# Optimization experiments

Measured on AMD Instinct MI355X. Metric: run time of the kernel, lower is better.

Reference implementation:

```python
import jax, jax.numpy as jnp
import numpy as np

NUM_HEADS = 16
HEAD_DIM = 80
HIDDEN = 1280
SEQ = 3072
NUM_SEGS = 6  # 6 packed images of 512 patches each


def rotate_half(x):
    x1, x2 = jnp.split(x, 2, axis=-1)
    return jnp.concatenate([-x2, x1], axis=-1)


def setup_inputs() -> dict:
    key = jax.random.key(0)
    ks = jax.random.split(key, 6)
    hidden_states = jax.random.normal(ks[0], (SEQ, HIDDEN), dtype=jnp.float32)
    # RoPE tables as in Qwen-VL vision: freqs over half the head_dim, duplicated
    half = HEAD_DIM // 2
    inv_freq = 1.0 / (10000.0 ** (jnp.arange(half, dtype=jnp.float32) / half))
    pos = jnp.arange(SEQ, dtype=jnp.float32)[:, None]
    freqs = pos * inv_freq[None, :]                      # (SEQ, half)
    emb = jnp.concatenate([freqs, freqs], axis=-1)       # (SEQ, HEAD_DIM)
    cos = jnp.cos(emb)
    sin = jnp.sin(emb)
    # Packed segment boundaries: [0, 512, 1024, ..., 3072]
    cu_seqlens = jnp.arange(0, SEQ + 1, SEQ // NUM_SEGS, dtype=jnp.int32)
    scale = 0.02
    w_qkv = jax.random.normal(ks[1], (3 * HIDDEN, HIDDEN), dtype=jnp.float32) * scale
    b_qkv = jax.random.normal(ks[2], (3 * HIDDEN,), dtype=jnp.float32) * scale
    w_proj = jax.random.normal(ks[3], (HIDDEN, HIDDEN), dtype=jnp.float32) * scale
    b_proj = jax.random.normal(ks[4], (HIDDEN,), dtype=jnp.float32) * scale
    return {
        "hidden_states": hidden_states, "cos": cos, "sin": sin,
        "w_qkv": w_qkv, "b_qkv": b_qkv, "w_proj": w_proj, "b_proj": b_proj,
        "cu_seqlens": cu_seqlens,
    }


def reference(hidden_states, cos, sin, w_qkv, b_qkv, w_proj, b_proj, cu_seqlens):
    S, H = hidden_states.shape
    nh, hd = NUM_HEADS, H // NUM_HEADS

    # Fused QKV projection: (S, 3H) -> q, k, v each (S, nh, hd)
    qkv = hidden_states @ w_qkv.T + b_qkv
    qkv = qkv.reshape(S, 3, nh, hd)
    q, k, v = qkv[:, 0], qkv[:, 1], qkv[:, 2]

    # Inline RoPE on q/k (cos/sin broadcast over heads)
    c = cos[:, None, :]
    s = sin[:, None, :]
    q = q * c + rotate_half(q) * s
    k = k * c + rotate_half(k) * s

    # Original casts fp32 -> fp16 for the flash attention kernel
    q16 = q.astype(jnp.float16)
    k16 = k.astype(jnp.float16)
    v16 = v.astype(jnp.float16)

    # Varlen masking: tokens attend only within their own packed segment
    tok = jnp.arange(S)
    seg = jnp.searchsorted(cu_seqlens, tok, side="right")  # (S,)
    same_seg = seg[:, None] == seg[None, :]                 # (S, S)

    scale = hd ** (-0.5)
    # Scores accumulated in fp32 (as flash attention does internally)
    scores = jnp.einsum("qhd,khd->hqk", q16, k16,
                        preferred_element_type=jnp.float32) * scale
    scores = jnp.where(same_seg[None], scores, jnp.finfo(jnp.float32).min)
    weights = jax.nn.softmax(scores, axis=-1).astype(jnp.float16)  # (nh, S, S)

    attn = jnp.einsum("hqk,khd->qhd", weights, v16)  # (S, nh, hd) fp16
    attn = attn.astype(jnp.float32).reshape(S, H)
    return attn @ w_proj.T + b_proj
```

## Files before the change

kernel.cpp:

```cpp
#include <hip/hip_runtime.h>

typedef _Float16 f16;
typedef _Float16 half8 __attribute__((ext_vector_type(8)));
typedef _Float16 half4 __attribute__((ext_vector_type(4)));
typedef float f32x4 __attribute__((ext_vector_type(4)));

__device__ __forceinline__ void gld_lds16(const void* g, void* l) {
  __builtin_amdgcn_global_load_lds((const __attribute__((address_space(1))) void*)g,
                                   (__attribute__((address_space(3))) void*)l, 16, 0, 0);
}

template <int CTRL>
__device__ __forceinline__ float dppf(float x) {
  return __builtin_bit_cast(float,
      __builtin_amdgcn_mov_dpp(__builtin_bit_cast(int, x), CTRL, 0xf, 0xf, true));
}
__device__ __forceinline__ float dpp_max16(float v) {
  v = fmaxf(v, dppf<0xB1>(v));
  v = fmaxf(v, dppf<0x4E>(v));
  v = fmaxf(v, dppf<0x128>(v));
  v = fmaxf(v, dppf<0x140>(v));
  return v;
}
__device__ __forceinline__ float dpp_sum16(float v) {
  v += dppf<0xB1>(v);
  v += dppf<0x4E>(v);
  v += dppf<0x128>(v);
  v += dppf<0x140>(v);
  return v;
}

__global__ void cvt_all(const float* __restrict__ hid, const float* __restrict__ wq,
                        const float* __restrict__ wp, f16* __restrict__ hid16,
                        f16* __restrict__ wq16, f16* __restrict__ wp16) {
  int b = blockIdx.x;
  const float* in;
  f16* out;
  int i;
  if (b < 3840) { in = hid; out = hid16; i = b * 256 + threadIdx.x; }
  else if (b < 8640) { in = wq; out = wq16; i = (b - 3840) * 256 + threadIdx.x; }
  else { in = wp; out = wp16; i = (b - 8640) * 256 + threadIdx.x; }
  float4 v = ((const float4*)in)[i];
  half4 o;
  o.x = (f16)v.x; o.y = (f16)v.y; o.z = (f16)v.z; o.w = (f16)v.w;
  ((half4*)out)[i] = o;
}

template <bool OUT_F16>
__global__ __launch_bounds__(256, 2) void gemm_bt(const f16* __restrict__ A,
                                                  const f16* __restrict__ B,
                                                  const float* __restrict__ bias,
                                                  void* __restrict__ Cout,
                                                  int K, int lda, int ldb, int ldc) {
  __shared__ f16 As[128 * 32];
  __shared__ f16 Bs[128 * 32];
  const int tid = threadIdx.x, lane = tid & 63, wave = tid >> 6;
  const int bm = blockIdx.x * 128, bn = blockIdx.y * 128;
  const int wm = (wave & 1) * 64, wn = (wave >> 1) * 64;
  const int lm = lane & 15, kq = (lane >> 4) * 8;
  const int arow = tid >> 2, acol = (tid & 3) * 8;

  const f16* Ab = A + (size_t)(bm + arow) * lda + acol;
  const f16* Bb = B + (size_t)(bn + arow) * ldb + acol;
  f16* AsW = As + wave * 512;
  f16* BsW = Bs + wave * 512;

  f32x4 acc[4][4] = {};
  for (int k0 = 0; k0 < K; k0 += 32) {
    gld_lds16(Ab + k0, AsW);
    gld_lds16(Ab + (size_t)64 * lda + k0, AsW + 2048);
    gld_lds16(Bb + k0, BsW);
    gld_lds16(Bb + (size_t)64 * ldb + k0, BsW + 2048);
    __syncthreads();
    half8 af[4], bf[4];
#pragma unroll
    for (int mt = 0; mt < 4; mt++) af[mt] = *(const half8*)&As[(wm + 16 * mt + lm) * 32 + kq];
#pragma unroll
    for (int nt = 0; nt < 4; nt++) bf[nt] = *(const half8*)&Bs[(wn + 16 * nt + lm) * 32 + kq];
#pragma unroll
    for (int mt = 0; mt < 4; mt++)
#pragma unroll
      for (int nt = 0; nt < 4; nt++)
        acc[mt][nt] = __builtin_amdgcn_mfma_f32_16x16x32_f16(af[mt], bf[nt], acc[mt][nt], 0, 0, 0);
    __syncthreads();
  }
  const int q4 = lane >> 4;
#pragma unroll
  for (int mt = 0; mt < 4; mt++)
#pragma unroll
    for (int nt = 0; nt < 4; nt++)
#pragma unroll
      for (int r = 0; r < 4; r++) {
        int gr = bm + wm + 16 * mt + 4 * q4 + r;
        int gc = bn + wn + 16 * nt + lm;
        float v = acc[mt][nt][r] + bias[gc];
        if (OUT_F16)
          ((f16*)Cout)[(size_t)gr * ldc + gc] = (f16)v;
        else
          ((float*)Cout)[(size_t)gr * ldc + gc] = v;
      }
}

template <bool OUT_F16>
__global__ __launch_bounds__(256, 2) void gemm_bt64(const f16* __restrict__ A,
                                                    const f16* __restrict__ B,
                                                    const float* __restrict__ bias,
                                                    void* __restrict__ Cout,
                                                    int K, int lda, int ldb, int ldc) {
  __shared__ f16 As[64 * 32];
  __shared__ f16 Bs[128 * 32];
  const int tid = threadIdx.x, lane = tid & 63, wave = tid >> 6;
  const int bm = blockIdx.x * 64, bn = blockIdx.y * 128;
  const int wm = (wave & 1) * 32, wn = (wave >> 1) * 64;
  const int lm = lane & 15, kq = (lane >> 4) * 8;
  const int arow = tid >> 2, acol = (tid & 3) * 8;

  const f16* Ab = A + (size_t)(bm + arow) * lda + acol;
  const f16* Bb = B + (size_t)(bn + arow) * ldb + acol;
  f16* AsW = As + wave * 512;
  f16* BsW = Bs + wave * 512;

  f32x4 acc[2][4] = {};
  for (int k0 = 0; k0 < K; k0 += 32) {
    gld_lds16(Ab + k0, AsW);
    gld_lds16(Bb + k0, BsW);
    gld_lds16(Bb + (size_t)64 * ldb + k0, BsW + 2048);
    __syncthreads();
    half8 af[2], bf[4];
#pragma unroll
    for (int mt = 0; mt < 2; mt++) af[mt] = *(const half8*)&As[(wm + 16 * mt + lm) * 32 + kq];
#pragma unroll
    for (int nt = 0; nt < 4; nt++) bf[nt] = *(const half8*)&Bs[(wn + 16 * nt + lm) * 32 + kq];
#pragma unroll
    for (int mt = 0; mt < 2; mt++)
#pragma unroll
      for (int nt = 0; nt < 4; nt++)
        acc[mt][nt] = __builtin_amdgcn_mfma_f32_16x16x32_f16(af[mt], bf[nt], acc[mt][nt], 0, 0, 0);
    __syncthreads();
  }
  const int q4 = lane >> 4;
#pragma unroll
  for (int mt = 0; mt < 2; mt++)
#pragma unroll
    for (int nt = 0; nt < 4; nt++)
#pragma unroll
      for (int r = 0; r < 4; r++) {
        int gr = bm + wm + 16 * mt + 4 * q4 + r;
        int gc = bn + wn + 16 * nt + lm;
        float v = acc[mt][nt][r] + bias[gc];
        if (OUT_F16)
          ((f16*)Cout)[(size_t)gr * ldc + gc] = (f16)v;
        else
          ((float*)Cout)[(size_t)gr * ldc + gc] = v;
      }
}

__global__ void rope_transpose(f16* __restrict__ qkv, const float* __restrict__ cosb,
                               const float* __restrict__ sinb, f16* __restrict__ vt) {
  __shared__ f16 tile[64][72];
  const int b = blockIdx.x;
  if (b < 1920) {
    int idx = b * 256 + threadIdx.x;
    int c = idx % 5;
    int t = idx / 5;
    int h = t % 16; t /= 16;
    int qk = t & 1;
    int s = t >> 1;
    size_t base = (size_t)s * 3840 + qk * 1280 + h * 80 + c * 8;
    half8 x = *(half8*)&qkv[base];
    half8 y = *(half8*)&qkv[base + 40];
    const float* cp = cosb + s * 80 + c * 8;
    const float* sp = sinb + s * 80 + c * 8;
    half8 ox, oy;
#pragma unroll
    for (int i = 0; i < 8; i++) {
      float cs = cp[i], sn = sp[i];
      float xf = (float)x[i], yf = (float)y[i];
      ox[i] = (f16)(xf * cs - yf * sn);
      oy[i] = (f16)(yf * cs + xf * sn);
    }
    *(half8*)&qkv[base] = ox;
    *(half8*)&qkv[base + 40] = oy;
  } else {
    const int bb = b - 1920;
    const int bs = (bb % 48) * 64;
    const int bd = (bb / 48) * 64;
    const int r = threadIdx.x >> 2, c = (threadIdx.x & 3) * 16;
    *(uint4*)&tile[r][c] = *(const uint4*)&qkv[(size_t)(bs + r) * 3840 + 2560 + bd + c];
    *(uint4*)&tile[r][c + 8] = *(const uint4*)&qkv[(size_t)(bs + r) * 3840 + 2560 + bd + c + 8];
    __syncthreads();
    f16 tmp[16];
#pragma unroll
    for (int i = 0; i < 16; i++) tmp[i] = tile[c + i][r];
    *(uint4*)&vt[(size_t)(bd + r) * 3072 + bs + c] = *(uint4*)&tmp[0];
    *(uint4*)&vt[(size_t)(bd + r) * 3072 + bs + c + 8] = *(uint4*)&tmp[8];
  }
}

__global__ __launch_bounds__(256, 4) void flash_attn5(const f16* __restrict__ qkv,
                                                      const f16* __restrict__ vt,
                                                      f16* __restrict__ attn) {
  __shared__ f16 S[20480];
  f16* Ks = S;
  f16* Vs = S + 10240;
  const int tid = threadIdx.x, lane = tid & 63, wave = tid >> 6;
  const int lm = lane & 15, q4 = lane >> 4;
  const int h = blockIdx.x, g = blockIdx.z;
  const int qbase = g * 512 + blockIdx.y * 64 + wave * 16;
  f16* P = S + wave * 2112;
  const half8 hz = {};

  const f16* qrow = qkv + (size_t)(qbase + lm) * 3840 + h * 80;
  half8 qf[3];
  qf[0] = *(const half8*)(qrow + q4 * 8);
  qf[1] = *(const half8*)(qrow + 32 + q4 * 8);
  qf[2] = (q4 < 2) ? *(const half8*)(qrow + 64 + q4 * 8) : hz;

  size_t kgo[5], vgo[5];
#pragma unroll
  for (int i = 0; i < 5; i++) {
    int t = (wave * 5 + i) * 1024 + lane * 16;
    int kr = t / 160, kcb = t % 160;
    kgo[i] = (size_t)(g * 512 + kr) * 3840 + 1280 + h * 80 + (kcb >> 1);
    int vd = t >> 8, vsb = t & 255;
    vgo[i] = (size_t)(h * 80 + vd) * 3072 + g * 512 + (vsb >> 1);
  }

  f32x4 oacc[5] = {};
  float mprev[4] = {-1e30f, -1e30f, -1e30f, -1e30f};
  float lsum[4] = {0.f, 0.f, 0.f, 0.f};
  const float sc = 0.11180339887498949f * 1.4426950408889634f;

  for (int j = 0; j < 4; j++) {
    __syncthreads();
#pragma unroll
    for (int i = 0; i < 5; i++) {
      int chunk = wave * 5 + i;
      gld_lds16(qkv + kgo[i] + (size_t)j * (128 * 3840), Ks + chunk * 512);
      gld_lds16(vt + vgo[i] + j * 128, Vs + chunk * 512);
    }
    __syncthreads();

    f32x4 sacc[8] = {};
#pragma unroll
    for (int ks = 0; ks < 3; ks++) {
      half8 bk[8];
#pragma unroll
      for (int nt = 0; nt < 8; nt++)
        bk[nt] = (ks < 2 || q4 < 2)
                     ? *(const half8*)&Ks[(16 * nt + lm) * 80 + 32 * ks + q4 * 8]
                     : hz;
#pragma unroll
      for (int nt = 0; nt < 8; nt++)
        sacc[nt] = __builtin_amdgcn_mfma_f32_16x16x32_f16(qf[ks], bk[nt], sacc[nt], 0, 0, 0);
    }

    float mnew[4], alpha[4], rs[4];
#pragma unroll
    for (int r = 0; r < 4; r++) {
      float v = fmaxf(fmaxf(fmaxf(sacc[0][r], sacc[1][r]), fmaxf(sacc[2][r], sacc[3][r])),
                      fmaxf(fmaxf(sacc[4][r], sacc[5][r]), fmaxf(sacc[6][r], sacc[7][r])));
      v = dpp_max16(v);
      mnew[r] = fmaxf(mprev[r], v * sc);
      alpha[r] = __builtin_exp2f(mprev[r] - mnew[r]);
      mprev[r] = mnew[r];
      rs[r] = 0.f;
    }
#pragma unroll
    for (int nt = 0; nt < 8; nt++)
#pragma unroll
      for (int r = 0; r < 4; r++) {
        float p = __builtin_exp2f(sacc[nt][r] * sc - mnew[r]);
        sacc[nt][r] = p;
        rs[r] += p;
      }
#pragma unroll
    for (int r = 0; r < 4; r++) {
      float v = dpp_sum16(rs[r]);
      lsum[r] = alpha[r] * lsum[r] + v;
#pragma unroll
      for (int nt2 = 0; nt2 < 5; nt2++) oacc[nt2][r] *= alpha[r];
    }

    __syncthreads();
#pragma unroll
    for (int nt = 0; nt < 8; nt++)
#pragma unroll
      for (int r = 0; r < 4; r++)
        P[(4 * q4 + r) * 132 + 16 * nt + lm] = (f16)sacc[nt][r];

#pragma unroll
    for (int ks = 0; ks < 4; ks++) {
      half8 ap = *(const half8*)&P[lm * 132 + ks * 32 + q4 * 8];
      half8 bv[5];
#pragma unroll
      for (int nt2 = 0; nt2 < 5; nt2++)
        bv[nt2] = *(const half8*)&Vs[(16 * nt2 + lm) * 128 + ks * 32 + q4 * 8];
#pragma unroll
      for (int nt2 = 0; nt2 < 5; nt2++)
        oacc[nt2] = __builtin_amdgcn_mfma_f32_16x16x32_f16(ap, bv[nt2], oacc[nt2], 0, 0, 0);
    }
  }
#pragma unroll
  for (int r = 0; r < 4; r++) {
    float inv = 1.0f / lsum[r];
    int s = qbase + 4 * q4 + r;
#pragma unroll
    for (int nt2 = 0; nt2 < 5; nt2++)
      attn[(size_t)s * 1280 + h * 80 + 16 * nt2 + lm] = (f16)(oacc[nt2][r] * inv);
  }
}

extern "C" void kernel_launch(void* const* d_in, const int* in_sizes, int n_in,
                              void* d_out, int out_size, void* d_ws, size_t ws_size,
                              hipStream_t stream) {
  const float* hidden = (const float*)d_in[0];
  const float* cosb   = (const float*)d_in[1];
  const float* sinb   = (const float*)d_in[2];
  const float* w_qkv  = (const float*)d_in[3];
  const float* b_qkv  = (const float*)d_in[4];
  const float* w_proj = (const float*)d_in[5];
  const float* b_proj = (const float*)d_in[6];

  char* ws = (char*)d_ws;
  f16* hidden16 = (f16*)(ws + 0);
  f16* wqkv16   = (f16*)(ws + 7864320);
  f16* wproj16  = (f16*)(ws + 17694720);
  f16* qkv16    = (f16*)(ws + 20971520);
  f16* attn16   = (f16*)(ws + 44564480);
  f16* vt16     = hidden16;

  cvt_all<<<10240, 256, 0, stream>>>(hidden, w_qkv, w_proj, hidden16, wqkv16, wproj16);

  gemm_bt<true><<<dim3(24, 30), 256, 0, stream>>>(hidden16, wqkv16, b_qkv, qkv16,
                                                  1280, 1280, 1280, 3840);

  rope_transpose<<<2880, 256, 0, stream>>>(qkv16, cosb, sinb, vt16);

  flash_attn5<<<dim3(16, 8, 6), 256, 0, stream>>>(qkv16, vt16, attn16);

  gemm_bt64<false><<<dim3(48, 10), 256, 0, stream>>>(attn16, wproj16, b_proj, d_out,
                                                     1280, 1280, 1280, 1280);
}
```

Baseline: 212.9 us.

## Replace QKV GEMM with 256x256-tile double-buffered pipelined kernel

Swaps the 128x128 QKV projection GEMM for a 512-thread kernel with 256x256 output tiles and 64-wide K steps. It double-buffers tiles in XOR-swizzled LDS and splits each K step into four quadrant phases. Each phase overlaps async global-to-LDS loads with MFMA work and raises wave priority during the math. The aim is more data reuse per tile, fewer LDS bank conflicts and hidden load latency. The cost is a grid of only 180 blocks, which may underfill the CUs, plus hardcoded dimensions and delicate barrier and waitcnt ordering.

```diff
diff --git a/kernel.cpp b/kernel.cpp
--- a/kernel.cpp
+++ b/kernel.cpp
@@ -46,59 +46,187 @@
   ((half4*)out)[i] = o;
 }
 
-template <bool OUT_F16>
-__global__ __launch_bounds__(256, 2) void gemm_bt(const f16* __restrict__ A,
+__global__ __launch_bounds__(512, 2) void gemm256(const f16* __restrict__ A,
                                                   const f16* __restrict__ B,
                                                   const float* __restrict__ bias,
-                                                  void* __restrict__ Cout,
-                                                  int K, int lda, int ldb, int ldc) {
-  __shared__ f16 As[128 * 32];
-  __shared__ f16 Bs[128 * 32];
-  const int tid = threadIdx.x, lane = tid & 63, wave = tid >> 6;
-  const int bm = blockIdx.x * 128, bn = blockIdx.y * 128;
-  const int wm = (wave & 1) * 64, wn = (wave >> 1) * 64;
-  const int lm = lane & 15, kq = (lane >> 4) * 8;
-  const int arow = tid >> 2, acol = (tid & 3) * 8;
-
-  const f16* Ab = A + (size_t)(bm + arow) * lda + acol;
-  const f16* Bb = B + (size_t)(bn + arow) * ldb + acol;
-  f16* AsW = As + wave * 512;
-  f16* BsW = Bs + wave * 512;
-
-  f32x4 acc[4][4] = {};
-  for (int k0 = 0; k0 < K; k0 += 32) {
-    gld_lds16(Ab + k0, AsW);
-    gld_lds16(Ab + (size_t)64 * lda + k0, AsW + 2048);
-    gld_lds16(Bb + k0, BsW);
-    gld_lds16(Bb + (size_t)64 * ldb + k0, BsW + 2048);
-    __syncthreads();
-    half8 af[4], bf[4];
-#pragma unroll
-    for (int mt = 0; mt < 4; mt++) af[mt] = *(const half8*)&As[(wm + 16 * mt + lm) * 32 + kq];
-#pragma unroll
-    for (int nt = 0; nt < 4; nt++) bf[nt] = *(const half8*)&Bs[(wn + 16 * nt + lm) * 32 + kq];
-#pragma unroll
-    for (int mt = 0; mt < 4; mt++)
-#pragma unroll
-      for (int nt = 0; nt < 4; nt++)
-        acc[mt][nt] = __builtin_amdgcn_mfma_f32_16x16x32_f16(af[mt], bf[nt], acc[mt][nt], 0, 0, 0);
-    __syncthreads();
-  }
-  const int q4 = lane >> 4;
-#pragma unroll
-  for (int mt = 0; mt < 4; mt++)
-#pragma unroll
-    for (int nt = 0; nt < 4; nt++)
-#pragma unroll
-      for (int r = 0; r < 4; r++) {
-        int gr = bm + wm + 16 * mt + 4 * q4 + r;
-        int gc = bn + wn + 16 * nt + lm;
-        float v = acc[mt][nt][r] + bias[gc];
-        if (OUT_F16)
-          ((f16*)Cout)[(size_t)gr * ldc + gc] = (f16)v;
-        else
-          ((float*)Cout)[(size_t)gr * ldc + gc] = v;
-      }
+                                                  f16* __restrict__ C) {
+  __shared__ f16 S[65536];
+  char* Sb = (char*)S;
+  const int tid = threadIdx.x, lane = tid & 63, wid = tid >> 6;
+  const int lm = lane & 15, q4 = lane >> 4;
+  const int wm = wid >> 2, wn = wid & 3;
+  const int bm = blockIdx.x * 256, bn = blockIdx.y * 256;
+  const int w2 = wid * 2048;
+
+  const int ch = ((lane & 7) ^ (lane >> 3)) << 3;
+  const int r0 = wid * 16 + (lane >> 3);
+  const int r1 = r0 + 8;
+  uint32_t aoff[2][2], boff[2][2];
+#pragma unroll
+  for (int h = 0; h < 2; h++) {
+    aoff[h][0] = (uint32_t)((bm + h * 64 + (r0 & 63) + ((r0 >> 6) << 7)) * 1280 + ch);
+    aoff[h][1] = (uint32_t)((bm + h * 64 + (r1 & 63) + ((r1 >> 6) << 7)) * 1280 + ch);
+    boff[h][0] = (uint32_t)((bn + h * 32 + (r0 & 31) + ((r0 >> 5) << 6)) * 1280 + ch);
+    boff[h][1] = (uint32_t)((bn + h * 32 + (r1 & 31) + ((r1 >> 5) << 6)) * 1280 + ch);
+  }
+
+  int aro[4][2], bro[2][2];
+#pragma unroll
+  for (int f = 0; f < 4; f++)
+#pragma unroll
+    for (int ks = 0; ks < 2; ks++) {
+      int row = wm * 64 + f * 16 + lm, colb = ks * 64 + q4 * 16;
+      aro[f][ks] = row * 128 + (colb ^ ((row & 7) << 4));
+    }
+#pragma unroll
+  for (int j = 0; j < 2; j++)
+#pragma unroll
+    for (int ks = 0; ks < 2; ks++) {
+      int row = wn * 32 + j * 16 + lm, colb = ks * 64 + q4 * 16;
+      bro[j][ks] = row * 128 + (colb ^ ((row & 7) << 4));
+    }
+
+  f32x4 acc[8][4] = {};
+
+  {
+    char* A0 = Sb;
+    char* B0 = Sb + 65536;
+    char* A1 = Sb + 32768;
+    char* B1 = Sb + 98304;
+    gld_lds16(A + aoff[0][0], A0 + w2);
+    gld_lds16(A + aoff[0][1], A0 + w2 + 1024);
+    gld_lds16(B + boff[1][0], B0 + 16384 + w2);
+    gld_lds16(B + boff[1][1], B0 + 16384 + w2 + 1024);
+    gld_lds16(A + aoff[1][0], A0 + 16384 + w2);
+    gld_lds16(A + aoff[1][1], A0 + 16384 + w2 + 1024);
+    gld_lds16(B + boff[0][0], B0 + w2);
+    gld_lds16(B + boff[0][1], B0 + w2 + 1024);
+    gld_lds16(A + aoff[0][0] + 64, A1 + w2);
+    gld_lds16(A + aoff[0][1] + 64, A1 + w2 + 1024);
+    gld_lds16(B + boff[1][0] + 64, B1 + 16384 + w2);
+    gld_lds16(B + boff[1][1] + 64, B1 + 16384 + w2 + 1024);
+    gld_lds16(A + aoff[1][0] + 64, A1 + 16384 + w2);
+    gld_lds16(A + aoff[1][1] + 64, A1 + 16384 + w2 + 1024);
+    asm volatile("s_waitcnt vmcnt(6)" ::: "memory");
+    __builtin_amdgcn_s_barrier();
+  }
+
+  constexpr int NT = 20;
+  half8 af[4][2], bf[2][2];
+  for (int t = 0; t < NT; ++t) {
+    const int p = t & 1;
+    char* Ab = Sb + p * 32768;
+    char* Bb = Sb + 65536 + p * 32768;
+    char* Bn = Sb + 65536 + (p ^ 1) * 32768;
+    const int k1 = (t + 1 < NT ? t + 1 : NT - 1) * 64;
+    const int k2 = (t + 2 < NT ? t + 2 : NT - 1) * 64;
+
+#pragma unroll
+    for (int f = 0; f < 4; f++) {
+      af[f][0] = *(const half8*)(Ab + aro[f][0]);
+      af[f][1] = *(const half8*)(Ab + aro[f][1]);
+    }
+#pragma unroll
+    for (int j = 0; j < 2; j++) {
+      bf[j][0] = *(const half8*)(Bb + bro[j][0]);
+      bf[j][1] = *(const half8*)(Bb + bro[j][1]);
+    }
+    gld_lds16(B + boff[0][0] + k1, Bn + w2);
+    gld_lds16(B + boff[0][1] + k1, Bn + w2 + 1024);
+    __builtin_amdgcn_s_barrier();
+    asm volatile("s_waitcnt lgkmcnt(0)" ::: "memory");
+    __builtin_amdgcn_sched_barrier(0);
+    __builtin_amdgcn_s_setprio(1);
+#pragma unroll
+    for (int ks = 0; ks < 2; ks++)
+#pragma unroll
+      for (int f = 0; f < 4; f++)
+#pragma unroll
+        for (int j = 0; j < 2; j++)
+          acc[f][j] =
+              __builtin_amdgcn_mfma_f32_16x16x32_f16(af[f][ks], bf[j][ks], acc[f][j], 0, 0, 0);
+    __builtin_amdgcn_s_setprio(0);
+    __builtin_amdgcn_s_barrier();
+
+#pragma unroll
+    for (int j = 0; j < 2; j++) {
+      bf[j][0] = *(const half8*)(Bb + 16384 + bro[j][0]);
+      bf[j][1] = *(const half8*)(Bb + 16384 + bro[j][1]);
+    }
+    gld_lds16(A + aoff[0][0] + k2, Ab + w2);
+    gld_lds16(A + aoff[0][1] + k2, Ab + w2 + 1024);
+    __builtin_amdgcn_s_barrier();
+    asm volatile("s_waitcnt lgkmcnt(0)" ::: "memory");
+    __builtin_amdgcn_sched_barrier(0);
+    __builtin_amdgcn_s_setprio(1);
+#pragma unroll
+    for (int ks = 0; ks < 2; ks++)
+#pragma unroll
+      for (int f = 0; f < 4; f++)
+#pragma unroll
+        for (int j = 0; j < 2; j++)
+          acc[f][2 + j] =
+              __builtin_amdgcn_mfma_f32_16x16x32_f16(af[f][ks], bf[j][ks], acc[f][2 + j], 0, 0, 0);
+    __builtin_amdgcn_s_setprio(0);
+    __builtin_amdgcn_s_barrier();
+
+#pragma unroll
+    for (int f = 0; f < 4; f++) {
+      af[f][0] = *(const half8*)(Ab + 16384 + aro[f][0]);
+      af[f][1] = *(const half8*)(Ab + 16384 + aro[f][1]);
+    }
+    gld_lds16(B + boff[1][0] + k2, Bb + 16384 + w2);
+    gld_lds16(B + boff[1][1] + k2, Bb + 16384 + w2 + 1024);
+    __builtin_amdgcn_s_barrier();
+    asm volatile("s_waitcnt lgkmcnt(0)" ::: "memory");
+    __builtin_amdgcn_sched_barrier(0);
+    __builtin_amdgcn_s_setprio(1);
+#pragma unroll
+    for (int ks = 0; ks < 2; ks++)
+#pragma unroll
+      for (int f = 0; f < 4; f++)
+#pragma unroll
+        for (int j = 0; j < 2; j++)
+          acc[4 + f][2 + j] = __builtin_amdgcn_mfma_f32_16x16x32_f16(af[f][ks], bf[j][ks],
+                                                                     acc[4 + f][2 + j], 0, 0, 0);
+    __builtin_amdgcn_s_setprio(0);
+    __builtin_amdgcn_s_barrier();
+
+#pragma unroll
+    for (int j = 0; j < 2; j++) {
+      bf[j][0] = *(const half8*)(Bb + bro[j][0]);
+      bf[j][1] = *(const half8*)(Bb + bro[j][1]);
+    }
+    gld_lds16(A + aoff[1][0] + k2, Ab + 16384 + w2);
+    gld_lds16(A + aoff[1][1] + k2, Ab + 16384 + w2 + 1024);
+    asm volatile("s_waitcnt vmcnt(6)" ::: "memory");
+    __builtin_amdgcn_s_barrier();
+    asm volatile("s_waitcnt lgkmcnt(0)" ::: "memory");
+    __builtin_amdgcn_sched_barrier(0);
+    __builtin_amdgcn_s_setprio(1);
+#pragma unroll
+    for (int ks = 0; ks < 2; ks++)
+#pragma unroll
+      for (int f = 0; f < 4; f++)
+#pragma unroll
+        for (int j = 0; j < 2; j++)
+          acc[4 + f][j] =
+              __builtin_amdgcn_mfma_f32_16x16x32_f16(af[f][ks], bf[j][ks], acc[4 + f][j], 0, 0, 0);
+    __builtin_amdgcn_s_setprio(0);
+    __builtin_amdgcn_s_barrier();
+  }
+
+#pragma unroll
+  for (int mf = 0; mf < 8; mf++)
+#pragma unroll
+    for (int nf = 0; nf < 4; nf++) {
+      const int gc = bn + wn * 64 + nf * 16 + lm;
+      const float bb = bias[gc];
+      const int gr0 = bm + wm * 128 + mf * 16 + q4 * 4;
+#pragma unroll
+      for (int r = 0; r < 4; r++)
+        C[(size_t)(gr0 + r) * 3840 + gc] = (f16)(acc[mf][nf][r] + bb);
+    }
 }
 
 template <bool OUT_F16>
@@ -332,8 +460,7 @@
 
   cvt_all<<<10240, 256, 0, stream>>>(hidden, w_qkv, w_proj, hidden16, wqkv16, wproj16);
 
-  gemm_bt<true><<<dim3(24, 30), 256, 0, stream>>>(hidden16, wqkv16, b_qkv, qkv16,
-                                                  1280, 1280, 1280, 3840);
+  gemm256<<<dim3(12, 15), 512, 0, stream>>>(hidden16, wqkv16, b_qkv, qkv16);
 
   rope_transpose<<<2880, 256, 0, stream>>>(qkv16, cosb, sinb, vt16);
 
```

Result: no change. 213.1 us (+0.1%).
